# Kernel optimization log

Hardware: AMD Instinct MI355X
Metric: run time of the kernel (lower is better)

## Reference

```python
import jax, jax.numpy as jnp
import numpy as np

THETA = 10000.0
D_K = 64
NUM_HEADS = 16


def _rope_tables(token_positions):
    # token_positions: [s] int -> cos/sin: [s, d_k//2]
    pos = token_positions.astype(jnp.float32)
    dim_idx = jnp.arange(0, D_K, 2, dtype=jnp.float32)
    freqs = 1.0 / (THETA ** (dim_idx / D_K))  # [d_k//2]
    ang = pos[:, None] * freqs[None, :]       # [s, d_k//2]
    return jnp.cos(ang), jnp.sin(ang)


def _apply_rope(x, cos, sin):
    # x: [b, h, s, d_k]; cos/sin: [s, d_k//2] broadcast over b, h
    x1 = x[..., 0::2]
    x2 = x[..., 1::2]
    r1 = x1 * cos - x2 * sin
    r2 = x2 * cos + x1 * sin
    return jnp.stack([r1, r2], axis=-1).reshape(x.shape)


def setup_inputs() -> dict:
    key = jax.random.key(0)
    ks = jax.random.split(key, 5)
    b, s, d = 2, 2048, 1024
    x = jax.random.normal(ks[0], (b, s, d), dtype=jnp.float32)
    token_positions = jnp.arange(s, dtype=jnp.int32)
    scale = (2.0 / (d + d)) ** 0.5
    Wq = jax.random.normal(ks[1], (d, d), dtype=jnp.float32) * scale
    Wk = jax.random.normal(ks[2], (d, d), dtype=jnp.float32) * scale
    Wv = jax.random.normal(ks[3], (d, d), dtype=jnp.float32) * scale
    Wo = jax.random.normal(ks[4], (d, d), dtype=jnp.float32) * scale
    return {"x": x, "token_positions": token_positions,
            "Wq": Wq, "Wk": Wk, "Wv": Wv, "Wo": Wo}


def reference(x, token_positions, Wq, Wk, Wv, Wo):
    b, s, d_model = x.shape
    h, d_k = NUM_HEADS, D_K

    def split_heads(t):
        return t.reshape(b, s, h, d_k).transpose(0, 2, 1, 3)  # [b, h, s, d_k]

    Q = split_heads(jnp.einsum('ij,bsj->bsi', Wq, x))
    K = split_heads(jnp.einsum('ij,bsj->bsi', Wk, x))
    V = split_heads(jnp.einsum('ij,bsj->bsi', Wv, x))

    cos, sin = _rope_tables(token_positions)
    Q = _apply_rope(Q, cos, sin)
    K = _apply_rope(K, cos, sin)

    scale = 1.0 / jnp.sqrt(jnp.float32(d_k))
    scores = jnp.einsum('bhqd,bhkd->bhqk', Q, K) * scale  # [b, h, s, s]
    causal = jnp.tril(jnp.ones((s, s), dtype=bool))
    scores = jnp.where(causal, scores, -jnp.inf)
    attn = jax.nn.softmax(scores, axis=-1)
    out = jnp.einsum('bhqk,bhkd->bhqd', attn, V)
    out = out.transpose(0, 2, 1, 3).reshape(b, s, d_model)
    return jnp.einsum('ij,bsj->bsi', Wo, out)
```

## Files before the change

kernel.cpp:

```cpp
#include <hip/hip_runtime.h>
#include <hip/hip_bf16.h>


typedef __attribute__((ext_vector_type(8))) __bf16 bf16x8;
typedef __attribute__((ext_vector_type(4))) float f32x4;
typedef __attribute__((ext_vector_type(16))) float f32x16;
typedef __attribute__((ext_vector_type(4))) int int4v;
typedef __attribute__((ext_vector_type(2))) unsigned int uint2v;

#define MFMA16(a, b, c) __builtin_amdgcn_mfma_f32_16x16x32_bf16(a, b, c, 0, 0, 0)
#define MFMA32(a, b, c) __builtin_amdgcn_mfma_f32_32x32x16_bf16(a, b, c, 0, 0, 0)

__device__ inline unsigned short f2b(float f) {
  unsigned u = __builtin_bit_cast(unsigned, f);
  u = (u + 0x7FFF + ((u >> 16) & 1)) >> 16;
  return (unsigned short)u;
}

__device__ inline unsigned pk2b(float lo, float hi) {
  return (unsigned)f2b(lo) | ((unsigned)f2b(hi) << 16);
}

__device__ inline unsigned cvtpk(float lo, float hi) {
  unsigned r;
  asm("v_cvt_pk_bf16_f32 %0, %1, %2" : "=v"(r) : "v"(lo), "v"(hi));
  return r;
}

__device__ inline void plswap(unsigned a, unsigned b, unsigned& o0, unsigned& o1) {
#if __has_builtin(__builtin_amdgcn_permlane32_swap)
  auto r = __builtin_amdgcn_permlane32_swap(a, b, false, false);
  o0 = r[0];
  o1 = r[1];
#else
  unsigned sa = (unsigned)__shfl_xor((int)a, 32, 64);
  unsigned sb = (unsigned)__shfl_xor((int)b, 32, 64);
  bool hi = (threadIdx.x & 32) != 0;
  o0 = hi ? sb : a;
  o1 = hi ? b : sa;
#endif
}

__device__ inline float fexp2(float x) {
#if __has_builtin(__builtin_amdgcn_exp2f)
  return __builtin_amdgcn_exp2f(x);
#else
  return exp2f(x);
#endif
}


__device__ inline void cvt4(const float* __restrict__ s, unsigned short* __restrict__ d,
                            int i, float sc) {
  float4 v = *(const float4*)(s + i);
  uint2v p = {pk2b(v.x * sc, v.y * sc), pk2b(v.z * sc, v.w * sc)};
  *(uint2v*)(d + i) = p;
}

__global__ __launch_bounds__(256) void prep_kernel(
    const float* __restrict__ x, const float* __restrict__ Wq,
    const float* __restrict__ Wk, const float* __restrict__ Wv,
    const float* __restrict__ Wo, const int* __restrict__ tp,
    unsigned short* __restrict__ xb, unsigned short* __restrict__ Wqkvb,
    unsigned short* __restrict__ Wob, float* __restrict__ cosT,
    float* __restrict__ sinT) {
  int t = blockIdx.x * 256 + threadIdx.x;
  if (t < 1048576) {
    cvt4(x, xb, t * 4, 1.0f);
  } else if (t < 1310720) {
    cvt4(Wq, Wqkvb, (t - 1048576) * 4, 0.18033688f);
  } else if (t < 1572864) {
    cvt4(Wk, Wqkvb + 1048576, (t - 1310720) * 4, 1.0f);
  } else if (t < 1835008) {
    cvt4(Wv, Wqkvb + 2097152, (t - 1572864) * 4, 1.0f);
  } else if (t < 2097152) {
    cvt4(Wo, Wob, (t - 1835008) * 4, 1.0f);
  } else {
    int base = (t - 2097152) * 4;
#pragma unroll
    for (int j = 0; j < 4; ++j) {
      int idx = base + j;
      int p = idx >> 5, i = idx & 31;
      float pos = (float)tp[p];
      float freq = powf(10000.0f, -(float)i / 32.0f);
      float ang = pos * freq;
      cosT[idx] = cosf(ang);
      sinT[idx] = sinf(ang);
    }
  }
}


__device__ __forceinline__ void g_stage(const unsigned short* __restrict__ A,
                                        const unsigned short* __restrict__ B,
                                        unsigned short* __restrict__ As,
                                        unsigned short* __restrict__ Bs,
                                        int m0, int n0, int k0, int w, int lane) {
  const int srow = lane >> 3;
  const int schunk = (lane & 7) ^ srow;
#pragma unroll
  for (int c = 0; c < 4; ++c) {
    const int rb = w * 32 + c * 8;
    const unsigned short* ga = A + (size_t)(m0 + rb + srow) * 1024 + k0 + schunk * 8;
    __builtin_amdgcn_global_load_lds(
        (const __attribute__((address_space(1))) void*)ga,
        (__attribute__((address_space(3))) void*)(As + rb * 64), 16, 0, 0);
    const int rl = rb + srow;
    const int rB = n0 + (rl & 96) + ((rl & 15) << 1) + ((rl >> 4) & 1);
    const unsigned short* gb = B + (size_t)rB * 1024 + k0 + schunk * 8;
    __builtin_amdgcn_global_load_lds(
        (const __attribute__((address_space(1))) void*)gb,
        (__attribute__((address_space(3))) void*)(Bs + rb * 64), 16, 0, 0);
  }
}


__global__ __launch_bounds__(256) void gemm_qkv_kernel(
    const unsigned short* __restrict__ A,
    const unsigned short* __restrict__ B,
    unsigned short* __restrict__ Qb, unsigned short* __restrict__ Kb,
    unsigned short* __restrict__ VbT,
    const float* __restrict__ cosT, const float* __restrict__ sinT) {
  __shared__ unsigned short As[2][128 * 64];
  __shared__ unsigned short Bs[2][128 * 64];
  const int bid = blockIdx.x;
  const int sw = (bid & 7) * 96 + (bid >> 3);
  const int n0 = (sw % 24) * 128, m0 = (sw / 24) * 128;
  const int tid = threadIdx.x, w = tid >> 6, lane = tid & 63;
  const int l15 = lane & 15, l4 = lane >> 4;
  const int wr = w >> 1, wc = w & 1;

  f32x4 acc[4][4] = {};

  g_stage(A, B, As[0], Bs[0], m0, n0, 0, w, lane);
  asm volatile("s_waitcnt vmcnt(0)" ::: "memory");
  __builtin_amdgcn_s_barrier();

  int cur = 0;
  for (int k0 = 0; k0 < 1024; k0 += 64) {
    if (k0 + 64 < 1024)
      g_stage(A, B, As[cur ^ 1], Bs[cur ^ 1], m0, n0, k0 + 64, w, lane);
#pragma unroll
    for (int kk = 0; kk < 2; ++kk) {
      bf16x8 af[4], bfr[4];
#pragma unroll
      for (int m = 0; m < 4; m++) {
        const int row = wr * 64 + m * 16 + l15;
        af[m] = *(const bf16x8*)(&As[cur][row * 64 + (((kk * 4 + l4) ^ (l15 & 7)) * 8)]);
      }
#pragma unroll
      for (int n = 0; n < 4; n++) {
        const int row = wc * 64 + n * 16 + l15;
        bfr[n] = *(const bf16x8*)(&Bs[cur][row * 64 + (((kk * 4 + l4) ^ (l15 & 7)) * 8)]);
      }
#pragma unroll
      for (int m = 0; m < 4; m++)
#pragma unroll
        for (int n = 0; n < 4; n++)
          acc[m][n] = MFMA16(af[m], bfr[n], acc[m][n]);
    }
    asm volatile("s_waitcnt vmcnt(0)" ::: "memory");
    __builtin_amdgcn_s_barrier();
    cur ^= 1;
  }

  const int cbase = n0 & 1023;
  if (n0 < 2048) {
    unsigned short* dst = (n0 < 1024) ? Qb : Kb;
#pragma unroll
    for (int m = 0; m < 4; m++) {
      const int row0 = m0 + wr * 64 + m * 16 + l4 * 4;
#pragma unroll
      for (int k = 0; k < 2; k++) {
        const int col = cbase + wc * 64 + k * 32 + 2 * l15;
        const int pi = k * 16 + l15;
#pragma unroll
        for (int r = 0; r < 4; r++) {
          const int pos = (row0 + r) & 2047;
          float c = cosT[pos * 32 + pi], s = sinT[pos * 32 + pi];
          float v0 = acc[m][2 * k][r], v1 = acc[m][2 * k + 1][r];
          float r1 = fmaf(v0, c, -v1 * s);
          float r2 = fmaf(v1, c, v0 * s);
          *(unsigned*)(dst + (size_t)(row0 + r) * 1024 + col) = pk2b(r1, r2);
        }
      }
    }
  } else {
#pragma unroll
    for (int m = 0; m < 4; m++) {
      const int row0 = m0 + wr * 64 + m * 16 + l4 * 4;
      const int bb = row0 >> 11, seq = row0 & 2047;
#pragma unroll
      for (int k = 0; k < 2; k++) {
        const int dkg = cbase + wc * 64 + k * 32 + 2 * l15;
        const int h = dkg >> 6, dk = dkg & 63;
        unsigned short* vp = VbT + (size_t)(bb * 16 + h) * 131072 + dk * 2048 + seq;
        uint2v e = {pk2b(acc[m][2 * k][0], acc[m][2 * k][1]),
                    pk2b(acc[m][2 * k][2], acc[m][2 * k][3])};
        *(uint2v*)vp = e;
        uint2v o = {pk2b(acc[m][2 * k + 1][0], acc[m][2 * k + 1][1]),
                    pk2b(acc[m][2 * k + 1][2], acc[m][2 * k + 1][3])};
        *(uint2v*)(vp + 2048) = o;
      }
    }
  }
}


__global__ __launch_bounds__(256) void gemm_out_kernel(
    const unsigned short* __restrict__ A,
    const unsigned short* __restrict__ B,
    float* __restrict__ out) {
  __shared__ unsigned short As[2][128 * 64];
  __shared__ unsigned short Bs[2][128 * 64];
  const int bid = blockIdx.x;
  const int sw = (bid & 7) * 32 + (bid >> 3);
  const int n0 = (sw % 8) * 128, m0 = (sw / 8) * 128;
  const int tid = threadIdx.x, w = tid >> 6, lane = tid & 63;
  const int l15 = lane & 15, l4 = lane >> 4;
  const int wr = w >> 1, wc = w & 1;

  f32x4 acc[4][4] = {};

  g_stage(A, B, As[0], Bs[0], m0, n0, 0, w, lane);
  asm volatile("s_waitcnt vmcnt(0)" ::: "memory");
  __builtin_amdgcn_s_barrier();

  int cur = 0;
  for (int k0 = 0; k0 < 1024; k0 += 64) {
    if (k0 + 64 < 1024)
      g_stage(A, B, As[cur ^ 1], Bs[cur ^ 1], m0, n0, k0 + 64, w, lane);
#pragma unroll
    for (int kk = 0; kk < 2; ++kk) {
      bf16x8 af[4], bfr[4];
#pragma unroll
      for (int m = 0; m < 4; m++) {
        const int row = wr * 64 + m * 16 + l15;
        af[m] = *(const bf16x8*)(&As[cur][row * 64 + (((kk * 4 + l4) ^ (l15 & 7)) * 8)]);
      }
#pragma unroll
      for (int n = 0; n < 4; n++) {
        const int row = wc * 64 + n * 16 + l15;
        bfr[n] = *(const bf16x8*)(&Bs[cur][row * 64 + (((kk * 4 + l4) ^ (l15 & 7)) * 8)]);
      }
#pragma unroll
      for (int m = 0; m < 4; m++)
#pragma unroll
        for (int n = 0; n < 4; n++)
          acc[m][n] = MFMA16(af[m], bfr[n], acc[m][n]);
    }
    asm volatile("s_waitcnt vmcnt(0)" ::: "memory");
    __builtin_amdgcn_s_barrier();
    cur ^= 1;
  }

#pragma unroll
  for (int m = 0; m < 4; m++) {
    const int row0 = m0 + wr * 64 + m * 16 + l4 * 4;
#pragma unroll
    for (int k = 0; k < 2; k++) {
      const int col = n0 + wc * 64 + k * 32 + 2 * l15;
#pragma unroll
      for (int r = 0; r < 4; r++) {
        float2 v = {acc[m][2 * k][r], acc[m][2 * k + 1][r]};
        *(float2*)(out + (size_t)(row0 + r) * 1024 + col) = v;
      }
    }
  }
}


__device__ __forceinline__ void stage_tiles(const unsigned short* __restrict__ Kgb,
                                            const unsigned short* __restrict__ Vgb,
                                            unsigned short* KsBuf, unsigned short* VsBuf,
                                            int kv0, int w, int lane) {
#pragma unroll
  for (int c = 0; c < 2; ++c) {
    const int rowbase = w * 16 + c * 8;
    const int row = rowbase + (lane >> 3);
    const int chunk = (lane & 7) ^ (lane >> 3);
    const unsigned short* gk = Kgb + (size_t)(kv0 + row) * 1024 + chunk * 8;
    __builtin_amdgcn_global_load_lds(
        (const __attribute__((address_space(1))) void*)gk,
        (__attribute__((address_space(3))) void*)(KsBuf + rowbase * 64), 16, 0, 0);
    const unsigned short* gv = Vgb + (size_t)row * 2048 + kv0 + chunk * 8;
    __builtin_amdgcn_global_load_lds(
        (const __attribute__((address_space(1))) void*)gv,
        (__attribute__((address_space(3))) void*)(VsBuf + rowbase * 64), 16, 0, 0);
  }
}

__device__ __forceinline__ void attn_chunk(
    int qt, int b, int h, int w, int lane,
    const unsigned short* __restrict__ Qb,
    const unsigned short* __restrict__ Kgb,
    const unsigned short* __restrict__ Vgb,
    unsigned short* __restrict__ Ob,
    unsigned short (*Ks)[64 * 64], unsigned short (*Vs)[64 * 64]) {
  const int l31 = lane & 31, l32 = lane >> 5;
  const int sw = l31 & 7;

  const unsigned short* qptr =
      Qb + (size_t)(b * 2048 + qt * 128 + w * 32 + l31) * 1024 + h * 64 + l32 * 8;
  bf16x8 qa[4];
#pragma unroll
  for (int kk = 0; kk < 4; ++kk) qa[kk] = *(const bf16x8*)(qptr + kk * 16);

  f32x16 oacc[2] = {};
  float m = -3e38f, l = 0.f;

  const int nt = 2 * qt + 2;
  stage_tiles(Kgb, Vgb, Ks[0], Vs[0], 0, w, lane);
  if (nt > 1) stage_tiles(Kgb, Vgb, Ks[1], Vs[1], 64, w, lane);

  int ib = 0, is_ = 2;
  for (int t = 0; t < nt; ++t) {
    if (t < nt - 1) {
      asm volatile("s_waitcnt vmcnt(4)" ::: "memory");
    } else {
      asm volatile("s_waitcnt vmcnt(0)" ::: "memory");
    }
    __builtin_amdgcn_s_barrier();
    __builtin_amdgcn_sched_barrier(0);
    if (t + 2 < nt)
      stage_tiles(Kgb, Vgb, Ks[is_], Vs[is_], (t + 2) * 64, w, lane);

    const char* ksb = (const char*)Ks[ib];
    f32x16 st[2];
#pragma unroll
    for (int f = 0; f < 2; ++f) {
      const char* kb = ksb + (f * 32 + l31) * 128;
      f32x16 z = {};
#pragma unroll
      for (int kk = 0; kk < 4; ++kk) {
        bf16x8 kf = *(const bf16x8*)(kb + ((((kk << 1) | l32) ^ sw) * 16));
        z = MFMA32(kf, qa[kk], z);
      }
      st[f] = z;
    }

    if (t >= 2 * qt + (w >> 1)) {
      const int qg = qt * 128 + w * 32 + l31;
      const int kvb = t * 64 + 4 * l32;
#pragma unroll
      for (int f = 0; f < 2; ++f)
#pragma unroll
        for (int reg = 0; reg < 16; ++reg) {
          int kv = kvb + 32 * f + (reg & 3) + 8 * (reg >> 2);
          if (kv > qg) st[f][reg] = -3e38f;
        }
    }

    float a8[8];
#pragma unroll
    for (int j = 0; j < 8; ++j)
      a8[j] = fmaxf(fmaxf(st[0][j], st[0][j + 8]), fmaxf(st[1][j], st[1][j + 8]));
    float pm = fmaxf(fmaxf(fmaxf(a8[0], a8[1]), fmaxf(a8[2], a8[3])),
                     fmaxf(fmaxf(a8[4], a8[5]), fmaxf(a8[6], a8[7])));
    pm = fmaxf(pm, __shfl_xor(pm, 32, 64));

    if (!__all(pm - m <= 8.0f)) {
      float mn = fmaxf(m, pm);
      float al = fexp2(m - mn);
      l *= al;
#pragma unroll
      for (int df = 0; df < 2; ++df)
#pragma unroll
        for (int reg = 0; reg < 16; ++reg) oacc[df][reg] *= al;
      m = mn;
    }

    unsigned pku[2][4][2];
    float rs0 = 0.f, rs1 = 0.f;
#pragma unroll
    for (int f = 0; f < 2; ++f)
#pragma unroll
      for (int rr = 0; rr < 4; ++rr)
#pragma unroll
        for (int i = 0; i < 2; ++i) {
          float p0 = fexp2(st[f][4 * rr + 2 * i] - m);
          float p1 = fexp2(st[f][4 * rr + 2 * i + 1] - m);
          rs0 += p0; rs1 += p1;
          pku[f][rr][i] = cvtpk(p0, p1);
        }
    float rs = rs0 + rs1;
    rs += __shfl_xor(rs, 32, 64);
    l += rs;

    union FB { unsigned u[4]; bf16x8 v; };
    FB pfrag[4];
#pragma unroll
    for (int kk = 0; kk < 4; ++kk) {
      const int f = kk >> 1, kl = kk & 1;
      unsigned o00, o10, o01, o11;
      plswap(pku[f][2 * kl][0], pku[f][2 * kl + 1][0], o00, o10);
      plswap(pku[f][2 * kl][1], pku[f][2 * kl + 1][1], o01, o11);
      pfrag[kk].u[0] = o00; pfrag[kk].u[1] = o01;
      pfrag[kk].u[2] = o10; pfrag[kk].u[3] = o11;
    }

    const char* vsb = (const char*)Vs[ib];
#pragma unroll
    for (int df = 0; df < 2; ++df) {
      const char* vb = vsb + (df * 32 + l31) * 128;
#pragma unroll
      for (int kk = 0; kk < 4; ++kk) {
        bf16x8 vf = *(const bf16x8*)(vb + ((((kk << 1) | l32) ^ sw) * 16));
        oacc[df] = MFMA32(vf, pfrag[kk].v, oacc[df]);
      }
    }

    ib = (ib == 2) ? 0 : ib + 1;
    is_ = (is_ == 2) ? 0 : is_ + 1;
  }

  const float inv = 1.0f / l;
  unsigned short* ob =
      Ob + (size_t)(b * 2048 + qt * 128 + w * 32 + l31) * 1024 + h * 64 + 4 * l32;
#pragma unroll
  for (int df = 0; df < 2; ++df)
#pragma unroll
    for (int rr = 0; rr < 4; ++rr)
#pragma unroll
      for (int i = 0; i < 2; ++i) {
        *(unsigned*)(ob + df * 32 + rr * 8 + 2 * i) =
            pk2b(oacc[df][4 * rr + 2 * i] * inv, oacc[df][4 * rr + 2 * i + 1] * inv);
      }
}

__global__ __launch_bounds__(256) void attn_kernel(
    const unsigned short* __restrict__ Qb,
    const unsigned short* __restrict__ Kb,
    const unsigned short* __restrict__ VbT,
    unsigned short* __restrict__ Ob) {
  __shared__ unsigned short Ks[3][64 * 64];
  __shared__ unsigned short Vs[3][64 * 64];
  const int bh = blockIdx.x;
  const int pair = blockIdx.y;
  const int b = bh >> 4, h = bh & 15;
  const int tid = threadIdx.x, w = tid >> 6, lane = tid & 63;

  const unsigned short* Kgb = Kb + (size_t)b * 2048 * 1024 + h * 64;
  const unsigned short* Vgb = VbT + (size_t)bh * 131072;

  attn_chunk(pair, b, h, w, lane, Qb, Kgb, Vgb, Ob, Ks, Vs);
  __syncthreads();
  attn_chunk(15 - pair, b, h, w, lane, Qb, Kgb, Vgb, Ob, Ks, Vs);
}


extern "C" void kernel_launch(void* const* d_in, const int* in_sizes, int n_in,
                              void* d_out, int out_size, void* d_ws, size_t ws_size,
                              hipStream_t stream) {
  (void)in_sizes; (void)n_in; (void)out_size; (void)ws_size;
  const float* x  = (const float*)d_in[0];
  const int*  tp  = (const int*)d_in[1];
  const float* Wq = (const float*)d_in[2];
  const float* Wk = (const float*)d_in[3];
  const float* Wv = (const float*)d_in[4];
  const float* Wo = (const float*)d_in[5];
  float* out = (float*)d_out;

  char* ws = (char*)d_ws;
  unsigned short* xb    = (unsigned short*)(ws);
  unsigned short* Ob    = (unsigned short*)(ws);
  unsigned short* Wqkvb = (unsigned short*)(ws + (8ull << 20));
  unsigned short* Wob   = (unsigned short*)(ws + (14ull << 20));
  unsigned short* Qb    = (unsigned short*)(ws + (16ull << 20));
  unsigned short* Kb    = (unsigned short*)(ws + (24ull << 20));
  unsigned short* VbT   = (unsigned short*)(ws + (32ull << 20));
  float* cosT = (float*)(ws + (40ull << 20));
  float* sinT = (float*)(ws + (40ull << 20) + 2048 * 32 * 4);

  prep_kernel<<<8256, 256, 0, stream>>>(x, Wq, Wk, Wv, Wo, tp, xb, Wqkvb, Wob, cosT, sinT);
  gemm_qkv_kernel<<<768, 256, 0, stream>>>(xb, Wqkvb, Qb, Kb, VbT, cosT, sinT);
  attn_kernel<<<dim3(32, 8), 256, 0, stream>>>(Qb, Kb, VbT, Ob);
  gemm_out_kernel<<<256, 256, 0, stream>>>(Ob, Wob, out);
}
```

Before: 119.2 us.

## Process paired query tiles jointly in one pass sharing K/V tile loads

Instead of running two sequential attention passes (query tile p, then 15-p), the kernel now keeps both query tiles' state in registers and streams K/V once over the longer range, reusing each staged K/V tile for both query tiles. This removes the duplicated K/V loads and pipeline restart for the shorter tile, and interleaves independent MFMA chains. In exchange it doubles accumulator and Q register usage, which can lower occupancy or cause spills. The QK MFMAs for tile A are still issued after its causal range ends, only softmax and PV are skipped.

```diff
diff --git a/kernel.cpp b/kernel.cpp
--- a/kernel.cpp
+++ b/kernel.cpp
@@ -290,130 +290,74 @@
   }
 }
 
-__device__ __forceinline__ void attn_chunk(
-    int qt, int b, int h, int w, int lane,
-    const unsigned short* __restrict__ Qb,
-    const unsigned short* __restrict__ Kgb,
-    const unsigned short* __restrict__ Vgb,
-    unsigned short* __restrict__ Ob,
-    unsigned short (*Ks)[64 * 64], unsigned short (*Vs)[64 * 64]) {
-  const int l31 = lane & 31, l32 = lane >> 5;
-  const int sw = l31 & 7;
-
-  const unsigned short* qptr =
-      Qb + (size_t)(b * 2048 + qt * 128 + w * 32 + l31) * 1024 + h * 64 + l32 * 8;
-  bf16x8 qa[4];
-#pragma unroll
-  for (int kk = 0; kk < 4; ++kk) qa[kk] = *(const bf16x8*)(qptr + kk * 16);
-
-  f32x16 oacc[2] = {};
-  float m = -3e38f, l = 0.f;
-
-  const int nt = 2 * qt + 2;
-  stage_tiles(Kgb, Vgb, Ks[0], Vs[0], 0, w, lane);
-  if (nt > 1) stage_tiles(Kgb, Vgb, Ks[1], Vs[1], 64, w, lane);
-
-  int ib = 0, is_ = 2;
-  for (int t = 0; t < nt; ++t) {
-    if (t < nt - 1) {
-      asm volatile("s_waitcnt vmcnt(4)" ::: "memory");
-    } else {
-      asm volatile("s_waitcnt vmcnt(0)" ::: "memory");
-    }
-    __builtin_amdgcn_s_barrier();
-    __builtin_amdgcn_sched_barrier(0);
-    if (t + 2 < nt)
-      stage_tiles(Kgb, Vgb, Ks[is_], Vs[is_], (t + 2) * 64, w, lane);
-
-    const char* ksb = (const char*)Ks[ib];
-    f32x16 st[2];
-#pragma unroll
-    for (int f = 0; f < 2; ++f) {
-      const char* kb = ksb + (f * 32 + l31) * 128;
-      f32x16 z = {};
-#pragma unroll
-      for (int kk = 0; kk < 4; ++kk) {
-        bf16x8 kf = *(const bf16x8*)(kb + ((((kk << 1) | l32) ^ sw) * 16));
-        z = MFMA32(kf, qa[kk], z);
-      }
-      st[f] = z;
-    }
-
-    if (t >= 2 * qt + (w >> 1)) {
-      const int qg = qt * 128 + w * 32 + l31;
-      const int kvb = t * 64 + 4 * l32;
-#pragma unroll
-      for (int f = 0; f < 2; ++f)
-#pragma unroll
-        for (int reg = 0; reg < 16; ++reg) {
-          int kv = kvb + 32 * f + (reg & 3) + 8 * (reg >> 2);
-          if (kv > qg) st[f][reg] = -3e38f;
-        }
-    }
-
-    float a8[8];
-#pragma unroll
-    for (int j = 0; j < 8; ++j)
-      a8[j] = fmaxf(fmaxf(st[0][j], st[0][j + 8]), fmaxf(st[1][j], st[1][j + 8]));
-    float pm = fmaxf(fmaxf(fmaxf(a8[0], a8[1]), fmaxf(a8[2], a8[3])),
-                     fmaxf(fmaxf(a8[4], a8[5]), fmaxf(a8[6], a8[7])));
-    pm = fmaxf(pm, __shfl_xor(pm, 32, 64));
-
-    if (!__all(pm - m <= 8.0f)) {
-      float mn = fmaxf(m, pm);
-      float al = fexp2(m - mn);
-      l *= al;
-#pragma unroll
-      for (int df = 0; df < 2; ++df)
-#pragma unroll
-        for (int reg = 0; reg < 16; ++reg) oacc[df][reg] *= al;
-      m = mn;
-    }
-
-    unsigned pku[2][4][2];
-    float rs0 = 0.f, rs1 = 0.f;
-#pragma unroll
-    for (int f = 0; f < 2; ++f)
-#pragma unroll
-      for (int rr = 0; rr < 4; ++rr)
-#pragma unroll
-        for (int i = 0; i < 2; ++i) {
-          float p0 = fexp2(st[f][4 * rr + 2 * i] - m);
-          float p1 = fexp2(st[f][4 * rr + 2 * i + 1] - m);
-          rs0 += p0; rs1 += p1;
-          pku[f][rr][i] = cvtpk(p0, p1);
-        }
-    float rs = rs0 + rs1;
-    rs += __shfl_xor(rs, 32, 64);
-    l += rs;
-
-    union FB { unsigned u[4]; bf16x8 v; };
-    FB pfrag[4];
-#pragma unroll
-    for (int kk = 0; kk < 4; ++kk) {
-      const int f = kk >> 1, kl = kk & 1;
-      unsigned o00, o10, o01, o11;
-      plswap(pku[f][2 * kl][0], pku[f][2 * kl + 1][0], o00, o10);
-      plswap(pku[f][2 * kl][1], pku[f][2 * kl + 1][1], o01, o11);
-      pfrag[kk].u[0] = o00; pfrag[kk].u[1] = o01;
-      pfrag[kk].u[2] = o10; pfrag[kk].u[3] = o11;
-    }
-
-    const char* vsb = (const char*)Vs[ib];
-#pragma unroll
-    for (int df = 0; df < 2; ++df) {
-      const char* vb = vsb + (df * 32 + l31) * 128;
-#pragma unroll
-      for (int kk = 0; kk < 4; ++kk) {
-        bf16x8 vf = *(const bf16x8*)(vb + ((((kk << 1) | l32) ^ sw) * 16));
-        oacc[df] = MFMA32(vf, pfrag[kk].v, oacc[df]);
-      }
-    }
-
-    ib = (ib == 2) ? 0 : ib + 1;
-    is_ = (is_ == 2) ? 0 : is_ + 1;
-  }
-
+struct PF { bf16x8 v[4]; };
+
+__device__ __forceinline__ void mask_st(f32x16* st, int qg, int kvb) {
+#pragma unroll
+  for (int f = 0; f < 2; ++f)
+#pragma unroll
+    for (int r = 0; r < 16; ++r) {
+      int kv = kvb + 32 * f + (r & 3) + 8 * (r >> 2);
+      if (kv > qg) st[f][r] = -3e38f;
+    }
+}
+
+__device__ __forceinline__ PF softmax_chunk(const f32x16* st, float& m, float& l,
+                                            f32x16* oacc) {
+  float a8[8];
+#pragma unroll
+  for (int j = 0; j < 8; ++j)
+    a8[j] = fmaxf(fmaxf(st[0][j], st[0][j + 8]), fmaxf(st[1][j], st[1][j + 8]));
+  float pm = fmaxf(fmaxf(fmaxf(a8[0], a8[1]), fmaxf(a8[2], a8[3])),
+                   fmaxf(fmaxf(a8[4], a8[5]), fmaxf(a8[6], a8[7])));
+  pm = fmaxf(pm, __shfl_xor(pm, 32, 64));
+
+  if (!__all(pm - m <= 8.0f)) {
+    float mn = fmaxf(m, pm);
+    float al = fexp2(m - mn);
+    l *= al;
+#pragma unroll
+    for (int df = 0; df < 2; ++df)
+#pragma unroll
+      for (int r = 0; r < 16; ++r) oacc[df][r] *= al;
+    m = mn;
+  }
+
+  unsigned pku[2][4][2];
+  float rs0 = 0.f, rs1 = 0.f;
+#pragma unroll
+  for (int f = 0; f < 2; ++f)
+#pragma unroll
+    for (int rr = 0; rr < 4; ++rr)
+#pragma unroll
+      for (int i = 0; i < 2; ++i) {
+        float p0 = fexp2(st[f][4 * rr + 2 * i] - m);
+        float p1 = fexp2(st[f][4 * rr + 2 * i + 1] - m);
+        rs0 += p0; rs1 += p1;
+        pku[f][rr][i] = cvtpk(p0, p1);
+      }
+  float rs = rs0 + rs1;
+  rs += __shfl_xor(rs, 32, 64);
+  l += rs;
+
+  union FB { unsigned u[4]; bf16x8 v; };
+  PF pf;
+#pragma unroll
+  for (int kk = 0; kk < 4; ++kk) {
+    const int f = kk >> 1, kl = kk & 1;
+    unsigned o00, o10, o01, o11;
+    plswap(pku[f][2 * kl][0], pku[f][2 * kl + 1][0], o00, o10);
+    plswap(pku[f][2 * kl][1], pku[f][2 * kl + 1][1], o01, o11);
+    FB fb;
+    fb.u[0] = o00; fb.u[1] = o01; fb.u[2] = o10; fb.u[3] = o11;
+    pf.v[kk] = fb.v;
+  }
+  return pf;
+}
+
+__device__ __forceinline__ void write_o(unsigned short* __restrict__ Ob, int b, int qt,
+                                        int w, int l31, int l32, int h,
+                                        const f32x16* oacc, float l) {
   const float inv = 1.0f / l;
   unsigned short* ob =
       Ob + (size_t)(b * 2048 + qt * 128 + w * 32 + l31) * 1024 + h * 64 + 4 * l32;
@@ -436,16 +380,106 @@
   __shared__ unsigned short Ks[3][64 * 64];
   __shared__ unsigned short Vs[3][64 * 64];
   const int bh = blockIdx.x;
-  const int pair = blockIdx.y;
+  const int p = blockIdx.y;
   const int b = bh >> 4, h = bh & 15;
   const int tid = threadIdx.x, w = tid >> 6, lane = tid & 63;
+  const int l31 = lane & 31, l32 = lane >> 5;
+  const int sw = l31 & 7;
+
+  const int qtA = p, qtB = 15 - p;
+  const int tdA = 2 * qtA + (w >> 1);
+  const int tdB = 2 * qtB + (w >> 1);
+  const int ntmax = 32 - 2 * p;
+  const int qgA = qtA * 128 + w * 32 + l31;
+  const int qgB = qtB * 128 + w * 32 + l31;
+
+  const unsigned short* qpA =
+      Qb + (size_t)(b * 2048 + qgA) * 1024 + h * 64 + l32 * 8;
+  const unsigned short* qpB =
+      Qb + (size_t)(b * 2048 + qgB) * 1024 + h * 64 + l32 * 8;
+  bf16x8 qaA[4], qaB[4];
+#pragma unroll
+  for (int kk = 0; kk < 4; ++kk) {
+    qaA[kk] = *(const bf16x8*)(qpA + kk * 16);
+    qaB[kk] = *(const bf16x8*)(qpB + kk * 16);
+  }
+
+  f32x16 oA[2] = {}, oB[2] = {};
+  float mA = -3e38f, lA = 0.f, mB = -3e38f, lB = 0.f;
 
   const unsigned short* Kgb = Kb + (size_t)b * 2048 * 1024 + h * 64;
   const unsigned short* Vgb = VbT + (size_t)bh * 131072;
 
-  attn_chunk(pair, b, h, w, lane, Qb, Kgb, Vgb, Ob, Ks, Vs);
-  __syncthreads();
-  attn_chunk(15 - pair, b, h, w, lane, Qb, Kgb, Vgb, Ob, Ks, Vs);
+  stage_tiles(Kgb, Vgb, Ks[0], Vs[0], 0, w, lane);
+  stage_tiles(Kgb, Vgb, Ks[1], Vs[1], 64, w, lane);
+
+  int ib = 0, is_ = 2;
+  for (int t = 0; t < ntmax; ++t) {
+    if (t < ntmax - 1) {
+      asm volatile("s_waitcnt vmcnt(4)" ::: "memory");
+    } else {
+      asm volatile("s_waitcnt vmcnt(0)" ::: "memory");
+    }
+    __builtin_amdgcn_s_barrier();
+    __builtin_amdgcn_sched_barrier(0);
+    if (t + 2 < ntmax)
+      stage_tiles(Kgb, Vgb, Ks[is_], Vs[is_], (t + 2) * 64, w, lane);
+
+    const bool aA = (t <= tdA), aB = (t <= tdB);
+
+    const char* ksb = (const char*)Ks[ib];
+    f32x16 sA[2], sB[2];
+#pragma unroll
+    for (int f = 0; f < 2; ++f) {
+      const char* kb = ksb + (f * 32 + l31) * 128;
+      f32x16 zA = {}, zB = {};
+#pragma unroll
+      for (int kk = 0; kk < 4; ++kk) {
+        bf16x8 kf = *(const bf16x8*)(kb + ((((kk << 1) | l32) ^ sw) * 16));
+        zB = MFMA32(kf, qaB[kk], zB);
+        zA = MFMA32(kf, qaA[kk], zA);
+      }
+      sA[f] = zA; sB[f] = zB;
+    }
+
+    const int kvb = t * 64 + 4 * l32;
+    if (t == tdA) mask_st(sA, qgA, kvb);
+    if (t == tdB) mask_st(sB, qgB, kvb);
+
+    PF pfA, pfB;
+    if (aA) pfA = softmax_chunk(sA, mA, lA, oA);
+    if (aB) pfB = softmax_chunk(sB, mB, lB, oB);
+
+    const char* vsb = (const char*)Vs[ib];
+    if (aA) {
+#pragma unroll
+      for (int df = 0; df < 2; ++df) {
+        const char* vb = vsb + (df * 32 + l31) * 128;
+#pragma unroll
+        for (int kk = 0; kk < 4; ++kk) {
+          bf16x8 vf = *(const bf16x8*)(vb + ((((kk << 1) | l32) ^ sw) * 16));
+          oB[df] = MFMA32(vf, pfB.v[kk], oB[df]);
+          oA[df] = MFMA32(vf, pfA.v[kk], oA[df]);
+        }
+      }
+    } else if (aB) {
+#pragma unroll
+      for (int df = 0; df < 2; ++df) {
+        const char* vb = vsb + (df * 32 + l31) * 128;
+#pragma unroll
+        for (int kk = 0; kk < 4; ++kk) {
+          bf16x8 vf = *(const bf16x8*)(vb + ((((kk << 1) | l32) ^ sw) * 16));
+          oB[df] = MFMA32(vf, pfB.v[kk], oB[df]);
+        }
+      }
+    }
+
+    ib = (ib == 2) ? 0 : ib + 1;
+    is_ = (is_ == 2) ? 0 : is_ + 1;
+  }
+
+  write_o(Ob, b, qtA, w, l31, l32, h, oA, lA);
+  write_o(Ob, b, qtB, w, l31, l32, h, oB, lB);
 }
 
 
```

New measurement: 141.8 us. 1.19x slower.
